# Kernel tuning notes

Measured on AMD Instinct MI355X. Metric: run time of the kernel, lower is better.

Reference implementation:

```python
import jax, jax.numpy as jnp
import numpy as np


def setup_inputs() -> dict:
    key = jax.random.key(0)
    ks = jax.random.split(key, 7)
    C, Cq = 128, 16  # channels, channels//8
    B, H, W = 8, 64, 64
    s = 0.05
    return {
        "x": jax.random.normal(ks[0], (B, C, H, W), jnp.float32),
        "wq": jax.random.normal(ks[1], (Cq, C), jnp.float32) * s,
        "bq": jnp.zeros((Cq,), jnp.float32),
        "wk": jax.random.normal(ks[2], (Cq, C), jnp.float32) * s,
        "bk": jnp.zeros((Cq,), jnp.float32),
        "wv": jax.random.normal(ks[3], (C, C), jnp.float32) * s,
        "bv": jnp.zeros((C,), jnp.float32),
    }


def reference(x, wq, bq, wk, bk, wv, bv):
    B, C, H, W = x.shape
    N = H * W
    dk = wq.shape[0]  # channels // 8
    xf = x.reshape(B, C, N)  # [B, C, N]
    # 1x1 convs == per-pixel linear maps over channels
    q = jnp.einsum('oc,bcn->bon', wq, xf) + bq[None, :, None]  # [B, dk, N]
    k = jnp.einsum('oc,bcn->bon', wk, xf) + bk[None, :, None]  # [B, dk, N]
    v = jnp.einsum('oc,bcn->bon', wv, xf) + bv[None, :, None]  # [B, C, N]
    # scores[b,i,j] = <q[:,i], k[:,j]> / sqrt(dk)
    scores = jnp.einsum('bdi,bdj->bij', q, k) / jnp.sqrt(jnp.asarray(dk, x.dtype))
    attn = jax.nn.softmax(scores, axis=-1)  # softmax over key dim j
    # out[b,c,i] = sum_j v[b,c,j] * attn[b,i,j]
    out = jnp.einsum('bcj,bij->bci', v, attn)
    return out.reshape(B, C, H, W) + x
```

## Files before the change

kernel.cpp:

```cpp
#include <hip/hip_runtime.h>
#include <hip/hip_bf16.h>

#define BATCH 8
#define CDIM  128
#define DK    16
#define NPIX  4096

typedef __attribute__((ext_vector_type(4)))  float    f32x4;
typedef __attribute__((ext_vector_type(16))) float    f32x16;
typedef __attribute__((ext_vector_type(8)))  short    s16x8;
typedef __attribute__((ext_vector_type(4)))  unsigned u32x4;

__device__ __forceinline__ short f2bf(float f) {
    union { float fv; unsigned u; } un; un.fv = f;
    unsigned r = un.u + 0x7FFFu + ((un.u >> 16) & 1u);
    return (short)(r >> 16);
}
__device__ __forceinline__ float bf2f(short s) {
    union { unsigned u; float f; } un; un.u = ((unsigned)(unsigned short)s) << 16;
    return un.f;
}
__device__ __forceinline__ float fexp2(float x) {
#if __has_builtin(__builtin_amdgcn_exp2f)
    return __builtin_amdgcn_exp2f(x);
#else
    return exp2f(x);
#endif
}
__device__ __forceinline__ unsigned pkbf(float lo, float hi) {
    __hip_bfloat162 h = __float22bfloat162_rn(make_float2(lo, hi));
    return *reinterpret_cast<unsigned*>(&h);
}
__device__ __forceinline__ f32x16 zero16() {
    f32x16 z;
    #pragma unroll
    for (int i = 0; i < 16; ++i) z[i] = 0.f;
    return z;
}

#define C2F 0.36067376022224085f
#define WPFRAGS (10 * 4 * 64)

__global__ __launch_bounds__(256) void wprep(
    const float* __restrict__ wq, const float* __restrict__ wk,
    const float* __restrict__ wv, short* __restrict__ Wp)
{
    const int mt   = blockIdx.x;
    const int t    = threadIdx.x;
    const int kt   = t >> 6;
    const int lane = t & 63;
    const int m    = mt * 16 + (lane & 15);
    const int c0   = kt * 32 + ((lane >> 4) << 3);

    const float* src; float scl = 1.f;
    if (m < 16)      { src = wq + m * CDIM; scl = C2F; }
    else if (m < 32) { src = wk + (m - 16) * CDIM; }
    else             { src = wv + (m - 32) * CDIM; }

    s16x8 frag;
    #pragma unroll
    for (int i = 0; i < 8; ++i) frag[i] = f2bf(src[c0 + i] * scl);
    *(s16x8*)(Wp + (((size_t)(mt * 4 + kt) * 64 + lane) << 3)) = frag;
}

__global__ __launch_bounds__(256) void qkv_proj(
    const float* __restrict__ x, const short* __restrict__ Wp,
    const float* __restrict__ bq, const float* __restrict__ bk,
    const float* __restrict__ bv,
    short* __restrict__ Qt, short* __restrict__ Kt, short* __restrict__ Vb)
{
    __shared__ __align__(16) short xb[64 * 128];

    const int tid   = threadIdx.x;
    const int bid   = blockIdx.x;
    const int b     = bid >> 6;
    const int nbase = (bid & 63) << 6;

    #pragma unroll
    for (int p = 0; p < 8; ++p) {
        const int c  = p * 16 + (tid >> 4);
        const int n4 = (tid & 15) << 2;
        float4 v = *(const float4*)(x + (((size_t)(b * CDIM + c)) << 12) + nbase + n4);
        unsigned u01 = pkbf(v.x, v.y);
        unsigned u23 = pkbf(v.z, v.w);
        const int ch = c >> 3, cl = c & 7;
        xb[(n4 + 0) * 128 + (((ch ^ ((n4 + 0) & 15)) << 3) | cl)] = (short)(u01 & 0xffffu);
        xb[(n4 + 1) * 128 + (((ch ^ ((n4 + 1) & 15)) << 3) | cl)] = (short)(u01 >> 16);
        xb[(n4 + 2) * 128 + (((ch ^ ((n4 + 2) & 15)) << 3) | cl)] = (short)(u23 & 0xffffu);
        xb[(n4 + 3) * 128 + (((ch ^ ((n4 + 3) & 15)) << 3) | cl)] = (short)(u23 >> 16);
    }
    __syncthreads();

    const int nt   = tid >> 6;
    const int lane = tid & 63;
    const int lo   = lane & 15;
    const int hi   = lane >> 4;
    const int n    = nt * 16 + lo;

    f32x4 acc[10];
    #pragma unroll
    for (int mt = 0; mt < 10; ++mt) { acc[mt][0]=0.f; acc[mt][1]=0.f; acc[mt][2]=0.f; acc[mt][3]=0.f; }

    #pragma unroll
    for (int kt = 0; kt < 4; ++kt) {
        const s16x8 bf = *(const s16x8*)&xb[n * 128 + (((kt * 4 + hi) ^ lo) << 3)];
        #pragma unroll
        for (int mt = 0; mt < 10; ++mt) {
            const s16x8 af = *(const s16x8*)(Wp + (((size_t)(mt * 4 + kt) * 64 + lane) << 3));
            acc[mt] = __builtin_amdgcn_mfma_f32_16x16x32_bf16(af, bf, acc[mt], 0, 0, 0);
        }
    }

    const int m4 = hi << 2;
    const int ng = nbase + n;
    {
        uint2 pk;
        pk.x = pkbf(acc[0][0] + bq[m4 + 0] * C2F, acc[0][1] + bq[m4 + 1] * C2F);
        pk.y = pkbf(acc[0][2] + bq[m4 + 2] * C2F, acc[0][3] + bq[m4 + 3] * C2F);
        *(uint2*)(Qt + ((((size_t)(b << 12)) + ng) << 4) + m4) = pk;
    }
    {
        uint2 pk;
        pk.x = pkbf(acc[1][0] + bk[m4 + 0], acc[1][1] + bk[m4 + 1]);
        pk.y = pkbf(acc[1][2] + bk[m4 + 2], acc[1][3] + bk[m4 + 3]);
        *(uint2*)(Kt + ((((size_t)(b << 12)) + ng) << 4) + m4) = pk;
    }
    #pragma unroll
    for (int mt = 2; mt < 10; ++mt) {
        #pragma unroll
        for (int r = 0; r < 4; ++r) {
            const int c = (mt - 2) * 16 + m4 + r;
            Vb[(((size_t)(b * CDIM + c)) << 12) + ng] = f2bf(acc[mt][r] + bv[c]);
        }
    }
}

template<int KSPLIT, bool DIRECT>
__global__ __launch_bounds__(256, 3) void attn_part(
    const short* __restrict__ Qt, const short* __restrict__ Kt,
    const short* __restrict__ Vb, const float* __restrict__ x,
    float* __restrict__ out, short* __restrict__ Op, float* __restrict__ lsum)
{
    constexpr int NKEY = NPIX / KSPLIT;
    constexpr int NT   = NKEY / 64;
    __shared__ __align__(16) short vs[CDIM * 64];

    const int tid = threadIdx.x;
    const int bid = blockIdx.x;
    const int qb  = bid & 31;
    const int kc  = (bid >> 5) % KSPLIT;
    const int b   = bid / (32 * KSPLIT);
    const int q0  = qb * 128 + (tid >> 6) * 32;
    const int l31 = tid & 31;
    const int hi2 = (tid >> 5) & 1;
    const int rx  = l31 & 7;
    const int kq  = hi2 << 3;
    const int pi  = (l31 & ~12) | ((l31 & 4) << 1) | ((l31 & 8) >> 1);

    const s16x8 qB = *(const s16x8*)(Qt + (((size_t)(b << 12) + q0 + l31) << 4) + kq);

    const int j8  = tid & 7;
    const int cb8 = tid >> 3;
    const short* vsrc = Vb + (((size_t)(b * CDIM + cb8)) << 12) + (j8 << 3);
    short* vdst = vs + cb8 * 64 + ((j8 ^ (cb8 & 7)) << 3);
    const size_t cstr = (size_t)32 << 12;

    const int jbase0 = kc * NKEY;
    const short* ktb = Kt + ((size_t)(b << 12) << 4);

    f32x16 O0 = zero16(), O1 = zero16(), O2 = zero16(), O3 = zero16();
    float l_acc = 0.f;

    s16x8 r0, r1, r2, r3;
    #define VLOAD(jb) do {                                   \
        r0 = *(const s16x8*)(vsrc + (jb));                   \
        r1 = *(const s16x8*)(vsrc + (jb) + cstr);            \
        r2 = *(const s16x8*)(vsrc + (jb) + 2 * cstr);        \
        r3 = *(const s16x8*)(vsrc + (jb) + 3 * cstr);        \
    } while (0)
    #define VSTORE() do {                                    \
        *(s16x8*)(vdst)           = r0;                      \
        *(s16x8*)(vdst + 32 * 64) = r1;                      \
        *(s16x8*)(vdst + 64 * 64) = r2;                      \
        *(s16x8*)(vdst + 96 * 64) = r3;                      \
    } while (0)
    #define LDSV(ct, ch) (*(const s16x8*)(vs + ((ct) * 32 + l31) * 64 + (((ch) ^ rx) << 3)))

    #define HALF(sv, jf, ktl) do {                                              \
        float p0 = fexp2(sv[8*(ktl)+0]), p1 = fexp2(sv[8*(ktl)+1]);            \
        float p2 = fexp2(sv[8*(ktl)+2]), p3 = fexp2(sv[8*(ktl)+3]);            \
        float p4 = fexp2(sv[8*(ktl)+4]), p5 = fexp2(sv[8*(ktl)+5]);            \
        float p6 = fexp2(sv[8*(ktl)+6]), p7 = fexp2(sv[8*(ktl)+7]);            \
        l_acc += ((p0+p1)+(p2+p3)) + ((p4+p5)+(p6+p7));                        \
        union { u32x4 u; s16x8 v; } pc_;                                       \
        pc_.u[0] = pkbf(p0,p1); pc_.u[1] = pkbf(p2,p3);                        \
        pc_.u[2] = pkbf(p4,p5); pc_.u[3] = pkbf(p6,p7);                        \
        const int ch_ = ((((jf)<<1) | (ktl)) << 1) | hi2;                       \
        __builtin_amdgcn_s_setprio(1);                                          \
        O0 = __builtin_amdgcn_mfma_f32_32x32x16_bf16(LDSV(0, ch_), pc_.v, O0, 0,0,0); \
        O1 = __builtin_amdgcn_mfma_f32_32x32x16_bf16(LDSV(1, ch_), pc_.v, O1, 0,0,0); \
        O2 = __builtin_amdgcn_mfma_f32_32x32x16_bf16(LDSV(2, ch_), pc_.v, O2, 0,0,0); \
        O3 = __builtin_amdgcn_mfma_f32_32x32x16_bf16(LDSV(3, ch_), pc_.v, O3, 0,0,0); \
        __builtin_amdgcn_s_setprio(0);                                          \
    } while (0)

    VLOAD(jbase0);
    VSTORE();
    __syncthreads();

    for (int t = 0; t < NT; ++t) {
        const int jb = jbase0 + (t << 6);
        if (t + 1 < NT) VLOAD(jb + 64);

        const s16x8 kA0 = *(const s16x8*)(ktb + (((size_t)(jb + pi)) << 4) + kq);
        const s16x8 kA1 = *(const s16x8*)(ktb + (((size_t)(jb + 32 + pi)) << 4) + kq);

        f32x16 s0 = __builtin_amdgcn_mfma_f32_32x32x16_bf16(kA0, qB, zero16(), 0, 0, 0);
        HALF(s0, 0, 0);
        HALF(s0, 0, 1);
        f32x16 s1 = __builtin_amdgcn_mfma_f32_32x32x16_bf16(kA1, qB, zero16(), 0, 0, 0);
        HALF(s1, 1, 0);
        HALF(s1, 1, 1);

        __syncthreads();
        if (t + 1 < NT) VSTORE();
        __syncthreads();
    }

    float l_tot = l_acc + __shfl_xor(l_acc, 32);
    const int ncol = q0 + l31;

    if constexpr (DIRECT) {
        const float inv = 1.f / l_tot;
        #define EPID(Ov, ct) do {                                              \
            _Pragma("unroll")                                                  \
            for (int r = 0; r < 16; ++r) {                                     \
                const int c = (ct)*32 + (r&3) + 8*(r>>2) + (hi2<<2);           \
                const size_t off = (((size_t)(b * CDIM + c)) << 12) + ncol;    \
                out[off] = Ov[r] * inv + x[off];                               \
            } } while (0)
        EPID(O0, 0); EPID(O1, 1); EPID(O2, 2); EPID(O3, 3);
    } else {
        const int prow = (kc * 8 + b) * CDIM;
        #define EPIP(Ov, ct) do {                                              \
            _Pragma("unroll")                                                  \
            for (int r = 0; r < 16; ++r) {                                     \
                const int c = (ct)*32 + (r&3) + 8*(r>>2) + (hi2<<2);           \
                Op[(((size_t)(prow + c)) << 12) + ncol] = f2bf(Ov[r]);         \
            } } while (0)
        EPIP(O0, 0); EPIP(O1, 1); EPIP(O2, 2); EPIP(O3, 3);
        if (!hi2) lsum[(((size_t)(kc * 8 + b)) << 12) + ncol] = l_tot;
    }
}

template<int KSPLIT>
__global__ __launch_bounds__(256) void attn_combine(
    const short* __restrict__ Op, const float* __restrict__ lsum,
    const float* __restrict__ x, float* __restrict__ out)
{
    __shared__ float linv[256];
    const int tid = threadIdx.x;
    const int bid = blockIdx.x;
    const int b   = bid >> 7;
    const int nb  = (bid >> 3) & 15;
    const int cb  = bid & 7;
    const int nbase = nb << 8;

    {
        float s = 0.f;
        #pragma unroll
        for (int k = 0; k < KSPLIT; ++k)
            s += lsum[(((size_t)(k * 8 + b)) << 12) + nbase + tid];
        linv[tid] = 1.f / s;
    }
    __syncthreads();

    const int n8 = (tid & 31) << 3;
    #pragma unroll
    for (int pass = 0; pass < 2; ++pass) {
        const int c = (cb << 4) + (pass << 3) + (tid >> 5);
        const size_t gbase = (((size_t)(b * CDIM + c)) << 12) + nbase + n8;
        float acc[8];
        #pragma unroll
        for (int j = 0; j < 8; ++j) acc[j] = 0.f;
        #pragma unroll
        for (int k = 0; k < KSPLIT; ++k) {
            s16x8 v = *(const s16x8*)(Op + (((size_t)((k * 8 + b) * CDIM + c)) << 12) + nbase + n8);
            #pragma unroll
            for (int j = 0; j < 8; ++j) acc[j] += bf2f(v[j]);
        }
        float4 li0 = *(const float4*)&linv[n8];
        float4 li1 = *(const float4*)&linv[n8 + 4];
        float4 x0  = *(const float4*)(x + gbase);
        float4 x1  = *(const float4*)(x + gbase + 4);
        float4 o0, o1;
        o0.x = acc[0] * li0.x + x0.x;  o0.y = acc[1] * li0.y + x0.y;
        o0.z = acc[2] * li0.z + x0.z;  o0.w = acc[3] * li0.w + x0.w;
        o1.x = acc[4] * li1.x + x1.x;  o1.y = acc[5] * li1.y + x1.y;
        o1.z = acc[6] * li1.z + x1.z;  o1.w = acc[7] * li1.w + x1.w;
        *(float4*)(out + gbase)     = o0;
        *(float4*)(out + gbase + 4) = o1;
    }
}

extern "C" void kernel_launch(void* const* d_in, const int* in_sizes, int n_in,
                              void* d_out, int out_size, void* d_ws, size_t ws_size,
                              hipStream_t stream) {
    const float* x  = (const float*)d_in[0];
    const float* wq = (const float*)d_in[1];
    const float* bq = (const float*)d_in[2];
    const float* wk = (const float*)d_in[3];
    const float* bk = (const float*)d_in[4];
    const float* wv = (const float*)d_in[5];
    const float* bv = (const float*)d_in[6];
    float* out = (float*)d_out;

    short* Qt = (short*)d_ws;
    short* Kt = Qt + (size_t)BATCH * NPIX * DK;
    short* Vw = Kt + (size_t)BATCH * NPIX * DK;
    short* Wpk = Vw + (size_t)BATCH * CDIM * NPIX;
    char*  extra = (char*)(Wpk + (size_t)WPFRAGS * 8);
    const size_t used    = (size_t)(extra - (char*)d_ws);
    const size_t opBytes = (size_t)BATCH * CDIM * NPIX * sizeof(short);
    const size_t lBytes  = (size_t)BATCH * NPIX * sizeof(float);

    wprep<<<dim3(10), dim3(256), 0, stream>>>(wq, wk, wv, Wpk);
    qkv_proj<<<dim3(512), dim3(256), 0, stream>>>(x, Wpk, bq, bk, bv, Qt, Kt, Vw);

    if (used + 4 * (opBytes + lBytes) <= ws_size) {
        short* Opw = (short*)extra;
        float* ls  = (float*)(extra + 4 * opBytes);
        attn_part<4, false><<<dim3(8 * 32 * 4), dim3(256), 0, stream>>>(Qt, Kt, Vw, x, out, Opw, ls);
        attn_combine<4><<<dim3(1024), dim3(256), 0, stream>>>(Opw, ls, x, out);
    } else if (used + 2 * (opBytes + lBytes) <= ws_size) {
        short* Opw = (short*)extra;
        float* ls  = (float*)(extra + 2 * opBytes);
        attn_part<2, false><<<dim3(8 * 32 * 2), dim3(256), 0, stream>>>(Qt, Kt, Vw, x, out, Opw, ls);
        attn_combine<2><<<dim3(1024), dim3(256), 0, stream>>>(Opw, ls, x, out);
    } else {
        attn_part<1, true><<<dim3(8 * 32), dim3(256), 0, stream>>>(Qt, Kt, Vw, x, out, nullptr, nullptr);
    }
}
```

Measured before the change: 82.16 us.

## Double-buffer V tiles and prefetch K; load x directly into MFMA fragments

The attention kernel now double-buffers the V tile in LDS, which removes one of the two barriers per key tile. It also prefetches the next K fragments into registers one iteration ahead, and raises the occupancy hint from 3 to 4 blocks. The projection kernel drops its LDS transpose staging and gathers x values straight from global memory into bf16 B-fragments. The V buffer doubles to 32KB per block, so LDS pressure and register pressure may limit the higher occupancy, and the strided per-channel loads of x may coalesce less well than the earlier float4 loads.

```diff
diff --git a/kernel.cpp b/kernel.cpp
--- a/kernel.cpp
+++ b/kernel.cpp
@@ -69,33 +69,36 @@
     const float* __restrict__ bv,
     short* __restrict__ Qt, short* __restrict__ Kt, short* __restrict__ Vb)
 {
-    __shared__ __align__(16) short xb[64 * 128];
-
     const int tid   = threadIdx.x;
     const int bid   = blockIdx.x;
     const int b     = bid >> 6;
     const int nbase = (bid & 63) << 6;
 
-    #pragma unroll
-    for (int p = 0; p < 8; ++p) {
-        const int c  = p * 16 + (tid >> 4);
-        const int n4 = (tid & 15) << 2;
-        float4 v = *(const float4*)(x + (((size_t)(b * CDIM + c)) << 12) + nbase + n4);
-        unsigned u01 = pkbf(v.x, v.y);
-        unsigned u23 = pkbf(v.z, v.w);
-        const int ch = c >> 3, cl = c & 7;
-        xb[(n4 + 0) * 128 + (((ch ^ ((n4 + 0) & 15)) << 3) | cl)] = (short)(u01 & 0xffffu);
-        xb[(n4 + 1) * 128 + (((ch ^ ((n4 + 1) & 15)) << 3) | cl)] = (short)(u01 >> 16);
-        xb[(n4 + 2) * 128 + (((ch ^ ((n4 + 2) & 15)) << 3) | cl)] = (short)(u23 & 0xffffu);
-        xb[(n4 + 3) * 128 + (((ch ^ ((n4 + 3) & 15)) << 3) | cl)] = (short)(u23 >> 16);
-    }
-    __syncthreads();
-
-    const int nt   = tid >> 6;
     const int lane = tid & 63;
     const int lo   = lane & 15;
     const int hi   = lane >> 4;
-    const int n    = nt * 16 + lo;
+    const int n    = ((tid >> 6) << 4) + lo;
+    const int ng   = nbase + n;
+
+    const float* xb = x + (((size_t)(b * CDIM)) << 12) + ng;
+
+    s16x8 bfr[4];
+    #pragma unroll
+    for (int kt = 0; kt < 4; ++kt) {
+        const float* xp = xb + (((size_t)(kt * 32 + hi * 8)) << 12);
+        float v0 = xp[0];
+        float v1 = xp[(size_t)1 << 12];
+        float v2 = xp[(size_t)2 << 12];
+        float v3 = xp[(size_t)3 << 12];
+        float v4 = xp[(size_t)4 << 12];
+        float v5 = xp[(size_t)5 << 12];
+        float v6 = xp[(size_t)6 << 12];
+        float v7 = xp[(size_t)7 << 12];
+        union { u32x4 u; s16x8 v; } pk;
+        pk.u[0] = pkbf(v0, v1); pk.u[1] = pkbf(v2, v3);
+        pk.u[2] = pkbf(v4, v5); pk.u[3] = pkbf(v6, v7);
+        bfr[kt] = pk.v;
+    }
 
     f32x4 acc[10];
     #pragma unroll
@@ -103,16 +106,14 @@
 
     #pragma unroll
     for (int kt = 0; kt < 4; ++kt) {
-        const s16x8 bf = *(const s16x8*)&xb[n * 128 + (((kt * 4 + hi) ^ lo) << 3)];
         #pragma unroll
         for (int mt = 0; mt < 10; ++mt) {
             const s16x8 af = *(const s16x8*)(Wp + (((size_t)(mt * 4 + kt) * 64 + lane) << 3));
-            acc[mt] = __builtin_amdgcn_mfma_f32_16x16x32_bf16(af, bf, acc[mt], 0, 0, 0);
+            acc[mt] = __builtin_amdgcn_mfma_f32_16x16x32_bf16(af, bfr[kt], acc[mt], 0, 0, 0);
         }
     }
 
     const int m4 = hi << 2;
-    const int ng = nbase + n;
     {
         uint2 pk;
         pk.x = pkbf(acc[0][0] + bq[m4 + 0] * C2F, acc[0][1] + bq[m4 + 1] * C2F);
@@ -136,14 +137,14 @@
 }
 
 template<int KSPLIT, bool DIRECT>
-__global__ __launch_bounds__(256, 3) void attn_part(
+__global__ __launch_bounds__(256, 4) void attn_part(
     const short* __restrict__ Qt, const short* __restrict__ Kt,
     const short* __restrict__ Vb, const float* __restrict__ x,
     float* __restrict__ out, short* __restrict__ Op, float* __restrict__ lsum)
 {
     constexpr int NKEY = NPIX / KSPLIT;
     constexpr int NT   = NKEY / 64;
-    __shared__ __align__(16) short vs[CDIM * 64];
+    __shared__ __align__(16) short vs[2][CDIM * 64];
 
     const int tid = threadIdx.x;
     const int bid = blockIdx.x;
@@ -162,7 +163,7 @@
     const int j8  = tid & 7;
     const int cb8 = tid >> 3;
     const short* vsrc = Vb + (((size_t)(b * CDIM + cb8)) << 12) + (j8 << 3);
-    short* vdst = vs + cb8 * 64 + ((j8 ^ (cb8 & 7)) << 3);
+    const int vdoff = cb8 * 64 + ((j8 ^ (cb8 & 7)) << 3);
     const size_t cstr = (size_t)32 << 12;
 
     const int jbase0 = kc * NKEY;
@@ -178,15 +179,17 @@
         r2 = *(const s16x8*)(vsrc + (jb) + 2 * cstr);        \
         r3 = *(const s16x8*)(vsrc + (jb) + 3 * cstr);        \
     } while (0)
-    #define VSTORE() do {                                    \
-        *(s16x8*)(vdst)           = r0;                      \
-        *(s16x8*)(vdst + 32 * 64) = r1;                      \
-        *(s16x8*)(vdst + 64 * 64) = r2;                      \
-        *(s16x8*)(vdst + 96 * 64) = r3;                      \
+    #define VSTORE(bufi) do {                                \
+        short* vd_ = &vs[bufi][vdoff];                       \
+        *(s16x8*)(vd_)           = r0;                       \
+        *(s16x8*)(vd_ + 32 * 64) = r1;                       \
+        *(s16x8*)(vd_ + 64 * 64) = r2;                       \
+        *(s16x8*)(vd_ + 96 * 64) = r3;                       \
     } while (0)
-    #define LDSV(ct, ch) (*(const s16x8*)(vs + ((ct) * 32 + l31) * 64 + (((ch) ^ rx) << 3)))
-
-    #define HALF(sv, jf, ktl) do {                                              \
+    #define KLOAD(jb) (*(const s16x8*)(ktb + (((size_t)((jb) + pi)) << 4) + kq))
+    #define LDSV(vb_, ct, ch) (*(const s16x8*)((vb_) + ((ct) * 32 + l31) * 64 + (((ch) ^ rx) << 3)))
+
+    #define HALF(sv, jf, ktl, vb_) do {                                         \
         float p0 = fexp2(sv[8*(ktl)+0]), p1 = fexp2(sv[8*(ktl)+1]);            \
         float p2 = fexp2(sv[8*(ktl)+2]), p3 = fexp2(sv[8*(ktl)+3]);            \
         float p4 = fexp2(sv[8*(ktl)+4]), p5 = fexp2(sv[8*(ktl)+5]);            \
@@ -197,33 +200,42 @@
         pc_.u[2] = pkbf(p4,p5); pc_.u[3] = pkbf(p6,p7);                        \
         const int ch_ = ((((jf)<<1) | (ktl)) << 1) | hi2;                       \
         __builtin_amdgcn_s_setprio(1);                                          \
-        O0 = __builtin_amdgcn_mfma_f32_32x32x16_bf16(LDSV(0, ch_), pc_.v, O0, 0,0,0); \
-        O1 = __builtin_amdgcn_mfma_f32_32x32x16_bf16(LDSV(1, ch_), pc_.v, O1, 0,0,0); \
-        O2 = __builtin_amdgcn_mfma_f32_32x32x16_bf16(LDSV(2, ch_), pc_.v, O2, 0,0,0); \
-        O3 = __builtin_amdgcn_mfma_f32_32x32x16_bf16(LDSV(3, ch_), pc_.v, O3, 0,0,0); \
+        O0 = __builtin_amdgcn_mfma_f32_32x32x16_bf16(LDSV(vb_, 0, ch_), pc_.v, O0, 0,0,0); \
+        O1 = __builtin_amdgcn_mfma_f32_32x32x16_bf16(LDSV(vb_, 1, ch_), pc_.v, O1, 0,0,0); \
+        O2 = __builtin_amdgcn_mfma_f32_32x32x16_bf16(LDSV(vb_, 2, ch_), pc_.v, O2, 0,0,0); \
+        O3 = __builtin_amdgcn_mfma_f32_32x32x16_bf16(LDSV(vb_, 3, ch_), pc_.v, O3, 0,0,0); \
         __builtin_amdgcn_s_setprio(0);                                          \
     } while (0)
 
     VLOAD(jbase0);
-    VSTORE();
+    s16x8 kA0c = KLOAD(jbase0);
+    s16x8 kA1c = KLOAD(jbase0 + 32);
+    VSTORE(0);
     __syncthreads();
 
     for (int t = 0; t < NT; ++t) {
-        const int jb = jbase0 + (t << 6);
-        if (t + 1 < NT) VLOAD(jb + 64);
-
-        const s16x8 kA0 = *(const s16x8*)(ktb + (((size_t)(jb + pi)) << 4) + kq);
-        const s16x8 kA1 = *(const s16x8*)(ktb + (((size_t)(jb + 32 + pi)) << 4) + kq);
-
-        f32x16 s0 = __builtin_amdgcn_mfma_f32_32x32x16_bf16(kA0, qB, zero16(), 0, 0, 0);
-        HALF(s0, 0, 0);
-        HALF(s0, 0, 1);
-        f32x16 s1 = __builtin_amdgcn_mfma_f32_32x32x16_bf16(kA1, qB, zero16(), 0, 0, 0);
-        HALF(s1, 1, 0);
-        HALF(s1, 1, 1);
-
-        __syncthreads();
-        if (t + 1 < NT) VSTORE();
+        const int jb  = jbase0 + (t << 6);
+        const int cur = t & 1;
+        const short* vcur = &vs[cur][0];
+
+        s16x8 kA0n, kA1n;
+        if (t + 1 < NT) {
+            VLOAD(jb + 64);
+            kA0n = KLOAD(jb + 64);
+            kA1n = KLOAD(jb + 96);
+        }
+
+        f32x16 s0 = __builtin_amdgcn_mfma_f32_32x32x16_bf16(kA0c, qB, zero16(), 0, 0, 0);
+        HALF(s0, 0, 0, vcur);
+        HALF(s0, 0, 1, vcur);
+        f32x16 s1 = __builtin_amdgcn_mfma_f32_32x32x16_bf16(kA1c, qB, zero16(), 0, 0, 0);
+        HALF(s1, 1, 0, vcur);
+        HALF(s1, 1, 1, vcur);
+
+        if (t + 1 < NT) {
+            VSTORE(cur ^ 1);
+            kA0c = kA0n; kA1c = kA1n;
+        }
         __syncthreads();
     }
 
```

New measurement: 95.13 us. +15.8%, slower.
